# Kernel tuning notes

Measured on AMD Instinct MI355X. Metric: run time of the kernel, lower is better.

Reference implementation:

```python
import jax, jax.numpy as jnp
import numpy as np

KS = 3   # kernel_size = sqrt(window_size=9)
PAD = 1  # KS // 2


def _unfold(t):
    # F.unfold(t, kernel_size=3, padding=1) then view(B,C,K,HW).permute(0,3,2,1)
    # -> (B, HW, K, C), K enumerated row-major over the 3x3 window.
    B, C, H, W = t.shape
    tp = jnp.pad(t, ((0, 0), (0, 0), (PAD, PAD), (PAD, PAD)))
    patches = jnp.stack(
        [tp[:, :, i:i + H, j:j + W] for i in range(KS) for j in range(KS)],
        axis=2,
    )  # (B, C, K, H, W)
    return patches.reshape(B, C, KS * KS, H * W).transpose(0, 3, 2, 1)


def setup_inputs() -> dict:
    key = jax.random.key(0)
    ks = jax.random.split(key, 8)
    B, C, H, W = 8, 256, 64, 64
    Cr = C // 8  # reduction=8
    return {
        "x": jax.random.normal(ks[0], (B, C, H, W), dtype=jnp.float32),
        "Wq": jax.random.normal(ks[1], (Cr, C), dtype=jnp.float32) * 0.02,
        "bq": jax.random.normal(ks[2], (Cr,), dtype=jnp.float32) * 0.02,
        "Wk": jax.random.normal(ks[3], (Cr, C), dtype=jnp.float32) * 0.02,
        "bk": jax.random.normal(ks[4], (Cr,), dtype=jnp.float32) * 0.02,
        "Wv": jax.random.normal(ks[5], (C, C), dtype=jnp.float32) * 0.02,
        "bv": jax.random.normal(ks[6], (C,), dtype=jnp.float32) * 0.02,
        "gamma": jax.random.normal(ks[7], (1,), dtype=jnp.float32) * 0.1,
    }


def reference(x, Wq, bq, Wk, bk, Wv, bv, gamma):
    B, C, H, W = x.shape
    # 1x1 convs == per-pixel linear projections
    q = jnp.einsum('bchw,oc->bohw', x, Wq) + bq[None, :, None, None]
    k = jnp.einsum('bchw,oc->bohw', x, Wk) + bk[None, :, None, None]
    v = jnp.einsum('bchw,oc->bohw', x, Wv) + bv[None, :, None, None]
    ku = _unfold(k)  # (B, HW, K, Cr)
    vu = _unfold(v)  # (B, HW, K, C)
    qf = q.reshape(B, -1, H * W).transpose(0, 2, 1)  # (B, HW, Cr)
    energy = jnp.einsum('bqc,bqkc->bqk', qf, ku)     # (B, HW, K)
    attn = jax.nn.softmax(energy, axis=-1)
    out = jnp.einsum('bqk,bqkc->bqc', attn, vu)      # (B, HW, C)
    out = out.transpose(0, 2, 1).reshape(B, C, H, W)
    return gamma * out + x
```

## Files before the change

### kernel.cpp

```cpp
#include <hip/hip_runtime.h>

#define HW   4096
#define HIMG 64
#define WIMG 64
#define CC   256
#define CR   32
#define B_   8

typedef __attribute__((ext_vector_type(8))) short bf16x8;
typedef __attribute__((ext_vector_type(4))) float f32x4;

__device__ inline unsigned short f2bf(float f) {
    union { float f; unsigned u; } v; v.f = f;
    return (unsigned short)((v.u + 0x8000u) >> 16);
}
__device__ inline float bf2f(unsigned short h) {
    union { unsigned u; float f; } v; v.u = ((unsigned)h) << 16; return v.f;
}
__device__ inline unsigned pack2(float a, float b) {
    return (unsigned)f2bf(a) | ((unsigned)f2bf(b) << 16);
}

__global__ __launch_bounds__(256) void wconv(
    const float* __restrict__ Wq, const float* __restrict__ bq,
    const float* __restrict__ Wk, const float* __restrict__ bk,
    const float* __restrict__ Wv, const float* __restrict__ bv,
    unsigned short* __restrict__ Wb, float* __restrict__ bb)
{
    const int o = blockIdx.x;
    const float* src; const float* bsrc; int orel;
    if (o < 32)      { src = Wq; bsrc = bq; orel = o;      }
    else if (o < 64) { src = Wk; bsrc = bk; orel = o - 32; }
    else             { src = Wv; bsrc = bv; orel = o - 64; }
    Wb[o * CC + threadIdx.x] = f2bf(src[orel * CC + threadIdx.x]);
    if (threadIdx.x == 0) bb[o] = bsrc[orel];
}

__global__ __launch_bounds__(256) void proj_gemm(
    const unsigned short* __restrict__ Wb, const float* __restrict__ bb,
    const float* __restrict__ x,
    float* __restrict__ q, float* __restrict__ k,
    unsigned short* __restrict__ vv)
{
    __shared__ unsigned short As[320 * 72];
    __shared__ float          xt32[64 * 65];
    __shared__ unsigned short Bs[64 * 64];

    const int b   = blockIdx.y;
    const int hw0 = blockIdx.x * 64;
    const int t    = threadIdx.x;
    const int lane = t & 63, wv = t >> 6;
    const int m16  = lane & 15, quad = lane >> 4;

    f32x4 acc[5][4];
    #pragma unroll
    for (int i = 0; i < 5; ++i)
        #pragma unroll
        for (int n = 0; n < 4; ++n)
            acc[i][n] = (f32x4){0.f, 0.f, 0.f, 0.f};

    for (int kc = 0; kc < 4; ++kc) {
        const int k0 = kc * 64;
        if (kc) __syncthreads();

        #pragma unroll
        for (int i = 0; i < 10; ++i) {
            int idx = t + 256 * i;
            int row = idx >> 3, s8 = idx & 7;
            *(uint4*)&As[row * 72 + s8 * 8] =
                *(const uint4*)&Wb[row * CC + k0 + s8 * 8];
        }
        #pragma unroll
        for (int i = 0; i < 4; ++i) {
            int idx = t + 256 * i;
            int c = idx >> 4, p4 = (idx & 15) * 4;
            float4 vx = *(const float4*)&x[((size_t)b * CC + k0 + c) * HW + hw0 + p4];
            *(float4*)&xt32[c * 65 + p4] = vx;
        }
        __syncthreads();

        {
            const int px = lane;
            const int c0 = wv * 16;
            float f[16];
            #pragma unroll
            for (int j = 0; j < 16; ++j)
                f[j] = xt32[(c0 + j) * 65 + px];
            uint4 w0, w1;
            w0.x = pack2(f[0],  f[1]);  w0.y = pack2(f[2],  f[3]);
            w0.z = pack2(f[4],  f[5]);  w0.w = pack2(f[6],  f[7]);
            w1.x = pack2(f[8],  f[9]);  w1.y = pack2(f[10], f[11]);
            w1.z = pack2(f[12], f[13]); w1.w = pack2(f[14], f[15]);
            const int lg0 = c0 >> 3, sw = px & 7;
            *(uint4*)&Bs[px * 64 + ((lg0     ^ sw) * 8)] = w0;
            *(uint4*)&Bs[px * 64 + (((lg0+1) ^ sw) * 8)] = w1;
        }
        __syncthreads();

        #pragma unroll
        for (int ks = 0; ks < 2; ++ks) {
            bf16x8 af[5], bf[4];
            #pragma unroll
            for (int i = 0; i < 5; ++i)
                af[i] = *(const bf16x8*)&As[((wv * 5 + i) * 16 + m16) * 72
                                            + ks * 32 + quad * 8];
            #pragma unroll
            for (int n = 0; n < 4; ++n) {
                int px = n * 16 + m16;
                int lg = ks * 4 + quad;
                bf[n] = *(const bf16x8*)&Bs[px * 64 + ((lg ^ (px & 7)) * 8)];
            }
            #pragma unroll
            for (int i = 0; i < 5; ++i)
                #pragma unroll
                for (int n = 0; n < 4; ++n)
                    acc[i][n] = __builtin_amdgcn_mfma_f32_16x16x32_bf16(
                        af[i], bf[n], acc[i][n], 0, 0, 0);
        }
    }

    #pragma unroll
    for (int i = 0; i < 5; ++i) {
        const int ob = (wv * 5 + i) * 16;
        #pragma unroll
        for (int r = 0; r < 4; ++r) {
            const int orow = quad * 4 + r;
            const float bias = bb[ob + orow];
            if (ob < 64) {
                float* dst = (ob < 32) ? q : k;
                int orel = (ob < 32) ? ob : ob - 32;
                size_t rowbase = ((size_t)b * CR + orel + orow) * HW;
                #pragma unroll
                for (int n = 0; n < 4; ++n)
                    dst[rowbase + hw0 + n * 16 + m16] = acc[i][n][r] + bias;
            } else {
                size_t rowbase = ((size_t)b * CC + (ob - 64) + orow) * HW;
                #pragma unroll
                for (int n = 0; n < 4; ++n)
                    vv[rowbase + hw0 + n * 16 + m16] = f2bf(acc[i][n][r] + bias);
            }
        }
    }
}

__global__ __launch_bounds__(512) void attn_apply(
    const float* __restrict__ q_, const float* __restrict__ k_,
    const unsigned short* __restrict__ vv,
    const float* __restrict__ x, const float* __restrict__ gamma,
    float* __restrict__ out)
{
    __shared__ union SM {
        struct { float qs[64][33]; float ks[3][64][33]; } e;
        unsigned short vs[3][128][72];
    } sm;
    __shared__ float es[64][9];
    __shared__ float aws[64][12];

    const int t  = threadIdx.x;
    const int hx = blockIdx.x;
    const int h  = ((hx & 7) << 3) | (hx >> 3);
    const int b  = blockIdx.y;

    {
        const int cr = t >> 4, p4 = (t & 15) * 4;
        float4 vq = *(const float4*)&q_[((size_t)b * CR + cr) * HW + h * WIMG + p4];
        sm.e.qs[p4 + 0][cr] = vq.x; sm.e.qs[p4 + 1][cr] = vq.y;
        sm.e.qs[p4 + 2][cr] = vq.z; sm.e.qs[p4 + 3][cr] = vq.w;
        #pragma unroll
        for (int r = 0; r < 3; ++r) {
            int hh = h + r - 1;
            float4 vk = make_float4(0.f, 0.f, 0.f, 0.f);
            if (hh >= 0 && hh < HIMG)
                vk = *(const float4*)&k_[((size_t)b * CR + cr) * HW + hh * WIMG + p4];
            sm.e.ks[r][p4 + 0][cr] = vk.x; sm.e.ks[r][p4 + 1][cr] = vk.y;
            sm.e.ks[r][p4 + 2][cr] = vk.z; sm.e.ks[r][p4 + 3][cr] = vk.w;
        }
    }
    __syncthreads();

    for (int id = t; id < 576; id += 512) {
        int px = id / 9, kk = id - px * 9;
        int di = kk / 3, dj = kk - di * 3;
        int hh = h + di - 1, ww = px + dj - 1;
        float e = 0.f;
        if (hh >= 0 && hh < HIMG && ww >= 0 && ww < WIMG) {
            float s = 0.f;
            #pragma unroll
            for (int c = 0; c < CR; ++c)
                s = fmaf(sm.e.qs[px][c], sm.e.ks[di][ww][c], s);
            e = s;
        }
        es[px][kk] = e;
    }
    __syncthreads();

    if (t < 64) {
        float m = es[t][0];
        #pragma unroll
        for (int kk = 1; kk < 9; ++kk) m = fmaxf(m, es[t][kk]);
        float ex[9]; float ssum = 0.f;
        #pragma unroll
        for (int kk = 0; kk < 9; ++kk) { ex[kk] = __expf(es[t][kk] - m); ssum += ex[kk]; }
        float inv = 1.f / ssum;
        #pragma unroll
        for (int kk = 0; kk < 9; ++kk) aws[t][kk] = ex[kk] * inv;
    }

    auto stage_v = [&](int cc) {
        #pragma unroll
        for (int i = 0; i < 12; ++i) {
            int idx = t + 512 * i;
            int p4 = (idx & 15) * 4;
            int c  = (idx >> 4) & 127;
            int r  = idx >> 11;
            int hh = h + r - 1;
            ushort4 u = make_ushort4(0, 0, 0, 0);
            if (hh >= 0 && hh < HIMG)
                u = *(const ushort4*)&vv[((size_t)b * CC + cc * 128 + c) * HW
                                          + hh * WIMG + p4];
            *(ushort4*)&sm.vs[r][c][4 + p4] = u;
        }
        if (t < 384) {
            int r = t >> 7, c = t & 127;
            ushort4 z = make_ushort4(0, 0, 0, 0);
            *(ushort4*)&sm.vs[r][c][0]  = z;
            *(ushort4*)&sm.vs[r][c][68] = z;
        }
    };

    stage_v(0);
    __syncthreads();

    const int px0 = (t & 15) * 4;
    const int cl  = t >> 4;
    const float g = gamma[0];
    float w[4][9];
    #pragma unroll
    for (int i = 0; i < 4; ++i)
        #pragma unroll
        for (int kk = 0; kk < 9; ++kk) w[i][kk] = aws[px0 + i][kk];

    #pragma unroll
    for (int cc = 0; cc < 2; ++cc) {
        if (cc) { __syncthreads(); stage_v(1); __syncthreads(); }
        #pragma unroll
        for (int ci = 0; ci < 4; ++ci) {
            int c = cl + 32 * ci;
            float a0 = 0.f, a1 = 0.f, a2 = 0.f, a3 = 0.f;
            #pragma unroll
            for (int r = 0; r < 3; ++r) {
                const unsigned short* row = &sm.vs[r][c][0];
                ushort4 uc = *(const ushort4*)&row[4 + px0];
                float c0 = bf2f(uc.x), c1 = bf2f(uc.y);
                float c2 = bf2f(uc.z), c3 = bf2f(uc.w);
                float lft = bf2f(row[3 + px0]);
                float rgt = bf2f(row[8 + px0]);
                int r3 = r * 3;
                a0 = fmaf(w[0][r3], lft, fmaf(w[0][r3+1], c0, fmaf(w[0][r3+2], c1, a0)));
                a1 = fmaf(w[1][r3], c0,  fmaf(w[1][r3+1], c1, fmaf(w[1][r3+2], c2, a1)));
                a2 = fmaf(w[2][r3], c1,  fmaf(w[2][r3+1], c2, fmaf(w[2][r3+2], c3, a2)));
                a3 = fmaf(w[3][r3], c2,  fmaf(w[3][r3+1], c3, fmaf(w[3][r3+2], rgt, a3)));
            }
            size_t base = ((size_t)b * CC + cc * 128 + c) * HW + h * WIMG + px0;
            float4 xa = *(const float4*)&x[base];
            float4 o;
            o.x = fmaf(g, a0, xa.x); o.y = fmaf(g, a1, xa.y);
            o.z = fmaf(g, a2, xa.z); o.w = fmaf(g, a3, xa.w);
            *(float4*)&out[base] = o;
        }
    }
}

extern "C" void kernel_launch(void* const* d_in, const int* in_sizes, int n_in,
                              void* d_out, int out_size, void* d_ws, size_t ws_size,
                              hipStream_t stream)
{
    const float* x     = (const float*)d_in[0];
    const float* Wq    = (const float*)d_in[1];
    const float* bq    = (const float*)d_in[2];
    const float* Wk    = (const float*)d_in[3];
    const float* bk    = (const float*)d_in[4];
    const float* Wv    = (const float*)d_in[5];
    const float* bv    = (const float*)d_in[6];
    const float* gamma = (const float*)d_in[7];
    float* out = (float*)d_out;

    float* q  = (float*)d_ws;
    float* k  = q + (size_t)B_ * CR * HW;
    unsigned short* vv = (unsigned short*)(k + (size_t)B_ * CR * HW);
    unsigned short* Wb = vv + (size_t)B_ * CC * HW;
    float* bb = (float*)(Wb + 320 * CC);

    wconv<<<dim3(320), 256, 0, stream>>>(Wq, bq, Wk, bk, Wv, bv, Wb, bb);
    proj_gemm<<<dim3(HW / 64, B_), 256, 0, stream>>>(Wb, bb, x, q, k, vv);
    attn_apply<<<dim3(HIMG, B_), 512, 0, stream>>>(q, k, vv, x, gamma, out);
}
```

Baseline: 135.4 us.

## Fuse projection GEMM and local attention into one kernel with halo recompute

Merges the projection GEMM and the attention-apply kernel into a single kernel. Each block computes q, k and v for its image row plus the rows above and below directly into shared memory, then runs the 3x3 softmax attention from LDS. This removes the global write and re-read of the q, k and bf16 v intermediates and one kernel launch. In exchange the GEMM work for k and v is done three times because of the halo rows, and the larger LDS footprint lowers occupancy.

Result: slower. 195.2 us (+44.1%).

```diff
diff --git a/kernel.cpp b/kernel.cpp
--- a/kernel.cpp
+++ b/kernel.cpp
@@ -36,27 +36,38 @@
     if (threadIdx.x == 0) bb[o] = bsrc[orel];
 }
 
-__global__ __launch_bounds__(256) void proj_gemm(
+__global__ __launch_bounds__(512) void fused(
     const unsigned short* __restrict__ Wb, const float* __restrict__ bb,
-    const float* __restrict__ x,
-    float* __restrict__ q, float* __restrict__ k,
-    unsigned short* __restrict__ vv)
+    const float* __restrict__ x, const float* __restrict__ gamma,
+    float* __restrict__ out)
 {
-    __shared__ unsigned short As[320 * 72];
-    __shared__ float          xt32[64 * 65];
-    __shared__ unsigned short Bs[64 * 64];
-
-    const int b   = blockIdx.y;
-    const int hw0 = blockIdx.x * 64;
+    struct P1 {
+        unsigned short As[320 * 72];
+        float          xt[64 * 196];
+        unsigned short Bs[192 * 64];
+    };
+    struct P2 {
+        unsigned short vL[3][256][72];
+        float          kL[3][64][33];
+        float          qL[64][33];
+        float          es[64][9];
+        float          aws[64][12];
+    };
+    __shared__ union SM { P1 p1; P2 p2; } sm;
+
     const int t    = threadIdx.x;
+    const int hx   = blockIdx.x;
+    const int h    = ((hx & 7) << 3) | (hx >> 3);
+    const int b    = blockIdx.y;
     const int lane = t & 63, wv = t >> 6;
     const int m16  = lane & 15, quad = lane >> 4;
-
-    f32x4 acc[5][4];
+    const int wm   = wv & 3, wn = wv >> 2;
+
+    f32x4 acc[5][6];
     #pragma unroll
     for (int i = 0; i < 5; ++i)
         #pragma unroll
-        for (int n = 0; n < 4; ++n)
+        for (int n = 0; n < 6; ++n)
             acc[i][n] = (f32x4){0.f, 0.f, 0.f, 0.f};
 
     for (int kc = 0; kc < 4; ++kc) {
@@ -64,117 +75,100 @@
         if (kc) __syncthreads();
 
         #pragma unroll
-        for (int i = 0; i < 10; ++i) {
-            int idx = t + 256 * i;
+        for (int i = 0; i < 5; ++i) {
+            int idx = t + 512 * i;
             int row = idx >> 3, s8 = idx & 7;
-            *(uint4*)&As[row * 72 + s8 * 8] =
+            *(uint4*)&sm.p1.As[row * 72 + s8 * 8] =
                 *(const uint4*)&Wb[row * CC + k0 + s8 * 8];
         }
         #pragma unroll
-        for (int i = 0; i < 4; ++i) {
-            int idx = t + 256 * i;
-            int c = idx >> 4, p4 = (idx & 15) * 4;
-            float4 vx = *(const float4*)&x[((size_t)b * CC + k0 + c) * HW + hw0 + p4];
-            *(float4*)&xt32[c * 65 + p4] = vx;
+        for (int i = 0; i < 6; ++i) {
+            int idx = t + 512 * i;
+            int c = idx / 48, f4 = idx % 48;
+            int p4 = f4 * 4;
+            int ri = p4 >> 6;
+            int hh = h + ri - 1;
+            float4 vx = make_float4(0.f, 0.f, 0.f, 0.f);
+            if (hh >= 0 && hh < HIMG)
+                vx = *(const float4*)&x[((size_t)b * CC + k0 + c) * HW
+                                         + hh * WIMG + (p4 & 63)];
+            *(float4*)&sm.p1.xt[c * 196 + p4] = vx;
         }
         __syncthreads();
 
-        {
-            const int px = lane;
-            const int c0 = wv * 16;
-            float f[16];
-            #pragma unroll
-            for (int j = 0; j < 16; ++j)
-                f[j] = xt32[(c0 + j) * 65 + px];
-            uint4 w0, w1;
-            w0.x = pack2(f[0],  f[1]);  w0.y = pack2(f[2],  f[3]);
-            w0.z = pack2(f[4],  f[5]);  w0.w = pack2(f[6],  f[7]);
-            w1.x = pack2(f[8],  f[9]);  w1.y = pack2(f[10], f[11]);
-            w1.z = pack2(f[12], f[13]); w1.w = pack2(f[14], f[15]);
-            const int lg0 = c0 >> 3, sw = px & 7;
-            *(uint4*)&Bs[px * 64 + ((lg0     ^ sw) * 8)] = w0;
-            *(uint4*)&Bs[px * 64 + (((lg0+1) ^ sw) * 8)] = w1;
+        #pragma unroll
+        for (int rep = 0; rep < 2; ++rep) {
+            int tk = wv + 8 * rep;
+            if (tk < 12) {
+                int px = (tk % 3) * 64 + lane;
+                int c0 = (tk / 3) * 16;
+                float f[16];
+                #pragma unroll
+                for (int j = 0; j < 16; ++j)
+                    f[j] = sm.p1.xt[(c0 + j) * 196 + px];
+                uint4 w0, w1;
+                w0.x = pack2(f[0],  f[1]);  w0.y = pack2(f[2],  f[3]);
+                w0.z = pack2(f[4],  f[5]);  w0.w = pack2(f[6],  f[7]);
+                w1.x = pack2(f[8],  f[9]);  w1.y = pack2(f[10], f[11]);
+                w1.z = pack2(f[12], f[13]); w1.w = pack2(f[14], f[15]);
+                const int lg0 = c0 >> 3, sw = px & 7;
+                *(uint4*)&sm.p1.Bs[px * 64 + ((lg0       ^ sw) * 8)] = w0;
+                *(uint4*)&sm.p1.Bs[px * 64 + (((lg0 + 1) ^ sw) * 8)] = w1;
+            }
         }
         __syncthreads();
 
         #pragma unroll
         for (int ks = 0; ks < 2; ++ks) {
-            bf16x8 af[5], bf[4];
+            bf16x8 af[5], bf[6];
             #pragma unroll
             for (int i = 0; i < 5; ++i)
-                af[i] = *(const bf16x8*)&As[((wv * 5 + i) * 16 + m16) * 72
-                                            + ks * 32 + quad * 8];
-            #pragma unroll
-            for (int n = 0; n < 4; ++n) {
-                int px = n * 16 + m16;
+                af[i] = *(const bf16x8*)&sm.p1.As[((wm * 5 + i) * 16 + m16) * 72
+                                                   + ks * 32 + quad * 8];
+            #pragma unroll
+            for (int n = 0; n < 6; ++n) {
+                int px = wn * 96 + n * 16 + m16;
                 int lg = ks * 4 + quad;
-                bf[n] = *(const bf16x8*)&Bs[px * 64 + ((lg ^ (px & 7)) * 8)];
+                bf[n] = *(const bf16x8*)&sm.p1.Bs[px * 64 + ((lg ^ (px & 7)) * 8)];
             }
             #pragma unroll
             for (int i = 0; i < 5; ++i)
                 #pragma unroll
-                for (int n = 0; n < 4; ++n)
+                for (int n = 0; n < 6; ++n)
                     acc[i][n] = __builtin_amdgcn_mfma_f32_16x16x32_bf16(
                         af[i], bf[n], acc[i][n], 0, 0, 0);
         }
     }
+    __syncthreads();
 
     #pragma unroll
     for (int i = 0; i < 5; ++i) {
-        const int ob = (wv * 5 + i) * 16;
+        const int ob = wm * 80 + i * 16;
         #pragma unroll
         for (int r = 0; r < 4; ++r) {
-            const int orow = quad * 4 + r;
-            const float bias = bb[ob + orow];
-            if (ob < 64) {
-                float* dst = (ob < 32) ? q : k;
-                int orel = (ob < 32) ? ob : ob - 32;
-                size_t rowbase = ((size_t)b * CR + orel + orow) * HW;
-                #pragma unroll
-                for (int n = 0; n < 4; ++n)
-                    dst[rowbase + hw0 + n * 16 + m16] = acc[i][n][r] + bias;
-            } else {
-                size_t rowbase = ((size_t)b * CC + (ob - 64) + orow) * HW;
-                #pragma unroll
-                for (int n = 0; n < 4; ++n)
-                    vv[rowbase + hw0 + n * 16 + m16] = f2bf(acc[i][n][r] + bias);
-            }
-        }
-    }
-}
-
-__global__ __launch_bounds__(512) void attn_apply(
-    const float* __restrict__ q_, const float* __restrict__ k_,
-    const unsigned short* __restrict__ vv,
-    const float* __restrict__ x, const float* __restrict__ gamma,
-    float* __restrict__ out)
-{
-    __shared__ union SM {
-        struct { float qs[64][33]; float ks[3][64][33]; } e;
-        unsigned short vs[3][128][72];
-    } sm;
-    __shared__ float es[64][9];
-    __shared__ float aws[64][12];
-
-    const int t  = threadIdx.x;
-    const int hx = blockIdx.x;
-    const int h  = ((hx & 7) << 3) | (hx >> 3);
-    const int b  = blockIdx.y;
-
-    {
-        const int cr = t >> 4, p4 = (t & 15) * 4;
-        float4 vq = *(const float4*)&q_[((size_t)b * CR + cr) * HW + h * WIMG + p4];
-        sm.e.qs[p4 + 0][cr] = vq.x; sm.e.qs[p4 + 1][cr] = vq.y;
-        sm.e.qs[p4 + 2][cr] = vq.z; sm.e.qs[p4 + 3][cr] = vq.w;
-        #pragma unroll
-        for (int r = 0; r < 3; ++r) {
-            int hh = h + r - 1;
-            float4 vk = make_float4(0.f, 0.f, 0.f, 0.f);
-            if (hh >= 0 && hh < HIMG)
-                vk = *(const float4*)&k_[((size_t)b * CR + cr) * HW + hh * WIMG + p4];
-            sm.e.ks[r][p4 + 0][cr] = vk.x; sm.e.ks[r][p4 + 1][cr] = vk.y;
-            sm.e.ks[r][p4 + 2][cr] = vk.z; sm.e.ks[r][p4 + 3][cr] = vk.w;
-        }
+            const int m = ob + quad * 4 + r;
+            const float bias = bb[m];
+            #pragma unroll
+            for (int n = 0; n < 6; ++n) {
+                int px = wn * 96 + n * 16 + m16;
+                int ri = px >> 6, ww = px & 63;
+                float val = acc[i][n][r] + bias;
+                if (m < CR) {
+                    if (ri == 1) sm.p2.qL[ww][m] = val;
+                } else if (m < 2 * CR) {
+                    sm.p2.kL[ri][ww][m - CR] = val;
+                } else {
+                    bool rv = (unsigned)(h + ri - 1) < (unsigned)HIMG;
+                    sm.p2.vL[ri][m - 2 * CR][4 + ww] =
+                        rv ? f2bf(val) : (unsigned short)0;
+                }
+            }
+        }
+    }
+    for (int p = t; p < 768; p += 512) {
+        int r = p >> 8, c = p & 255;
+        *(ushort4*)&sm.p2.vL[r][c][0]  = make_ushort4(0, 0, 0, 0);
+        *(ushort4*)&sm.p2.vL[r][c][68] = make_ushort4(0, 0, 0, 0);
     }
     __syncthreads();
 
@@ -187,69 +181,46 @@
             float s = 0.f;
             #pragma unroll
             for (int c = 0; c < CR; ++c)
-                s = fmaf(sm.e.qs[px][c], sm.e.ks[di][ww][c], s);
+                s = fmaf(sm.p2.qL[px][c], sm.p2.kL[di][ww][c], s);
             e = s;
         }
-        es[px][kk] = e;
+        sm.p2.es[px][kk] = e;
     }
     __syncthreads();
 
     if (t < 64) {
-        float m = es[t][0];
-        #pragma unroll
-        for (int kk = 1; kk < 9; ++kk) m = fmaxf(m, es[t][kk]);
+        float m = sm.p2.es[t][0];
+        #pragma unroll
+        for (int kk = 1; kk < 9; ++kk) m = fmaxf(m, sm.p2.es[t][kk]);
         float ex[9]; float ssum = 0.f;
         #pragma unroll
-        for (int kk = 0; kk < 9; ++kk) { ex[kk] = __expf(es[t][kk] - m); ssum += ex[kk]; }
+        for (int kk = 0; kk < 9; ++kk) {
+            ex[kk] = __expf(sm.p2.es[t][kk] - m);
+            ssum += ex[kk];
+        }
         float inv = 1.f / ssum;
         #pragma unroll
-        for (int kk = 0; kk < 9; ++kk) aws[t][kk] = ex[kk] * inv;
-    }
-
-    auto stage_v = [&](int cc) {
-        #pragma unroll
-        for (int i = 0; i < 12; ++i) {
-            int idx = t + 512 * i;
-            int p4 = (idx & 15) * 4;
-            int c  = (idx >> 4) & 127;
-            int r  = idx >> 11;
-            int hh = h + r - 1;
-            ushort4 u = make_ushort4(0, 0, 0, 0);
-            if (hh >= 0 && hh < HIMG)
-                u = *(const ushort4*)&vv[((size_t)b * CC + cc * 128 + c) * HW
-                                          + hh * WIMG + p4];
-            *(ushort4*)&sm.vs[r][c][4 + p4] = u;
-        }
-        if (t < 384) {
-            int r = t >> 7, c = t & 127;
-            ushort4 z = make_ushort4(0, 0, 0, 0);
-            *(ushort4*)&sm.vs[r][c][0]  = z;
-            *(ushort4*)&sm.vs[r][c][68] = z;
-        }
-    };
-
-    stage_v(0);
-    __syncthreads();
-
-    const int px0 = (t & 15) * 4;
-    const int cl  = t >> 4;
-    const float g = gamma[0];
-    float w[4][9];
-    #pragma unroll
-    for (int i = 0; i < 4; ++i)
-        #pragma unroll
-        for (int kk = 0; kk < 9; ++kk) w[i][kk] = aws[px0 + i][kk];
-
-    #pragma unroll
-    for (int cc = 0; cc < 2; ++cc) {
-        if (cc) { __syncthreads(); stage_v(1); __syncthreads(); }
-        #pragma unroll
-        for (int ci = 0; ci < 4; ++ci) {
+        for (int kk = 0; kk < 9; ++kk) sm.p2.aws[t][kk] = ex[kk] * inv;
+    }
+    __syncthreads();
+
+    {
+        const int px0 = (t & 15) * 4;
+        const int cl  = t >> 4;
+        const float g = gamma[0];
+        float w[4][9];
+        #pragma unroll
+        for (int i = 0; i < 4; ++i)
+            #pragma unroll
+            for (int kk = 0; kk < 9; ++kk) w[i][kk] = sm.p2.aws[px0 + i][kk];
+
+        #pragma unroll
+        for (int ci = 0; ci < 8; ++ci) {
             int c = cl + 32 * ci;
             float a0 = 0.f, a1 = 0.f, a2 = 0.f, a3 = 0.f;
             #pragma unroll
             for (int r = 0; r < 3; ++r) {
-                const unsigned short* row = &sm.vs[r][c][0];
+                const unsigned short* row = &sm.p2.vL[r][c][0];
                 ushort4 uc = *(const ushort4*)&row[4 + px0];
                 float c0 = bf2f(uc.x), c1 = bf2f(uc.y);
                 float c2 = bf2f(uc.z), c3 = bf2f(uc.w);
@@ -261,7 +232,7 @@
                 a2 = fmaf(w[2][r3], c1,  fmaf(w[2][r3+1], c2, fmaf(w[2][r3+2], c3, a2)));
                 a3 = fmaf(w[3][r3], c2,  fmaf(w[3][r3+1], c3, fmaf(w[3][r3+2], rgt, a3)));
             }
-            size_t base = ((size_t)b * CC + cc * 128 + c) * HW + h * WIMG + px0;
+            size_t base = ((size_t)b * CC + c) * HW + h * WIMG + px0;
             float4 xa = *(const float4*)&x[base];
             float4 o;
             o.x = fmaf(g, a0, xa.x); o.y = fmaf(g, a1, xa.y);
@@ -285,13 +256,9 @@
     const float* gamma = (const float*)d_in[7];
     float* out = (float*)d_out;
 
-    float* q  = (float*)d_ws;
-    float* k  = q + (size_t)B_ * CR * HW;
-    unsigned short* vv = (unsigned short*)(k + (size_t)B_ * CR * HW);
-    unsigned short* Wb = vv + (size_t)B_ * CC * HW;
+    unsigned short* Wb = (unsigned short*)d_ws;
     float* bb = (float*)(Wb + 320 * CC);
 
     wconv<<<dim3(320), 256, 0, stream>>>(Wq, bq, Wk, bk, Wv, bv, Wb, bb);
-    proj_gemm<<<dim3(HW / 64, B_), 256, 0, stream>>>(Wb, bb, x, q, k, vv);
-    attn_apply<<<dim3(HIMG, B_), 512, 0, stream>>>(q, k, vv, x, gamma, out);
-}
+    fused<<<dim3(HIMG, B_), 512, 0, stream>>>(Wb, bb, x, gamma, out);
+}
```
